# Kernel tuning notes

Hardware: AMD Instinct MI355X
Metric: run time of the kernel (lower is better)

The kernel has to match this reference:

```python
import itertools
import jax, jax.numpy as jnp
import numpy as np

DIM = 448
HEADS = 8
KEY_DIM = 32
ATTN_RATIO = 4
RES = 7
N = RES * RES  # 49 tokens
D_V = KEY_DIM * ATTN_RATIO  # 128
DH = D_V * HEADS  # 1024
H_QKV = DH + 2 * KEY_DIM * HEADS  # 1536
HIDDEN = 4 * DIM  # 1792
SCALE = KEY_DIM ** -0.5
LS_INIT = 1e-05
B = 1024


def _build_bias_idx():
    points = list(itertools.product(range(RES), range(RES)))
    offsets = {}
    idxs = []
    for p1 in points:
        for p2 in points:
            off = (abs(p1[0] - p2[0]), abs(p1[1] - p2[1]))
            if off not in offsets:
                offsets[off] = len(offsets)
            idxs.append(offsets[off])
    return np.array(idxs, dtype=np.int32).reshape(N, N), len(offsets)


def setup_inputs() -> dict:
    key = jax.random.key(0)
    ks = jax.random.split(key, 16)
    bias_idx_np, n_off = _build_bias_idx()
    s = lambda fan: 1.0 / np.sqrt(fan)
    return {
        "x": jax.random.normal(ks[0], (B, N, DIM), jnp.float32),
        "qkv_w": jax.random.normal(ks[1], (H_QKV, DIM), jnp.float32) * s(DIM),
        "qkv_b": jnp.zeros((H_QKV,), jnp.float32),
        "proj_w": jax.random.normal(ks[2], (DIM, DH), jnp.float32) * s(DH),
        "proj_b": jnp.zeros((DIM,), jnp.float32),
        "fc1_w": jax.random.normal(ks[3], (HIDDEN, DIM), jnp.float32) * s(DIM),
        "fc1_b": jnp.zeros((HIDDEN,), jnp.float32),
        "fc2_w": jax.random.normal(ks[4], (DIM, HIDDEN), jnp.float32) * s(HIDDEN),
        "fc2_b": jnp.zeros((DIM,), jnp.float32),
        "norm1_g": jnp.ones((DIM,), jnp.float32),
        "norm1_b": jnp.zeros((DIM,), jnp.float32),
        "norm2_g": jnp.ones((DIM,), jnp.float32),
        "norm2_b": jnp.zeros((DIM,), jnp.float32),
        "ls1_gamma": jnp.full((DIM,), LS_INIT, jnp.float32),
        "ls2_gamma": jnp.full((DIM,), LS_INIT, jnp.float32),
        "attn_biases": jax.random.normal(ks[5], (HEADS, n_off), jnp.float32) * 0.02,
        "bias_idx": jnp.asarray(bias_idx_np),
    }


def _ln(x, g, b, eps=1e-5):
    mu = jnp.mean(x, axis=-1, keepdims=True)
    var = jnp.mean(jnp.square(x - mu), axis=-1, keepdims=True)
    return (x - mu) * jax.lax.rsqrt(var + eps) * g + b


def reference(x, qkv_w, qkv_b, proj_w, proj_b, fc1_w, fc1_b, fc2_w, fc2_b,
              norm1_g, norm1_b, norm2_g, norm2_b, ls1_gamma, ls2_gamma,
              attn_biases, bias_idx):
    Bk, Nk, C = x.shape
    # --- token mixer: attention with gathered relative-position bias ---
    h = _ln(x, norm1_g, norm1_b)
    qkv = (h @ qkv_w.T + qkv_b).reshape(Bk, Nk, HEADS, -1)
    q, k, v = jnp.split(qkv, [KEY_DIM, 2 * KEY_DIM], axis=3)
    # scores: [B, H, N, N]
    attn = jnp.einsum('bnhd,bmhd->bhnm', q, k) * SCALE
    attn = attn + attn_biases[:, bias_idx]  # gather bias [H, N, N]
    attn = jax.nn.softmax(attn, axis=-1)
    out = jnp.einsum('bhnm,bmhd->bnhd', attn, v).reshape(Bk, Nk, DH)
    out = out @ proj_w.T + proj_b
    x = x + out * ls1_gamma
    # --- MLP ---
    h2 = _ln(x, norm2_g, norm2_b)
    h2 = jax.nn.gelu(h2 @ fc1_w.T + fc1_b, approximate=False)
    h2 = h2 @ fc2_w.T + fc2_b
    x = x + h2 * ls2_gamma
    return x
```

## Files before the change

### kernel.cpp

```cpp
#include <hip/hip_runtime.h>
#include <hip/hip_bf16.h>
#include <hip/hip_fp8.h>


#define NTOK 49
#define CDIM 448
#define NHEAD 8
#define DHID 1024
#define HQKV 1536
#define FHID 1792
#define QK_SCALE 0.1767766952966369f
#define INV_SCALE 5.656854249492381f

typedef __attribute__((ext_vector_type(8))) short bf16x8;
typedef __attribute__((ext_vector_type(4))) float f32x4;
typedef unsigned int u32;
typedef unsigned char u8;

__device__ __forceinline__ short f2b(float f) {
    __hip_bfloat16 h = __float2bfloat16(f);
    return *reinterpret_cast<short*>(&h);
}
__device__ __forceinline__ u8 f2f8(float f) {
    __hip_fp8_e4m3 h(f);
    return *reinterpret_cast<u8*>(&h);
}

__device__ __forceinline__ void gll16(const void* g, void* l) {
    __builtin_amdgcn_global_load_lds(
        (const __attribute__((address_space(1))) u32*)g,
        (__attribute__((address_space(3))) u32*)l, 16, 0, 0);
}

__global__ __launch_bounds__(256) void convert_w(
    const float* __restrict__ s0, const float* __restrict__ s1,
    const float* __restrict__ s2, const float* __restrict__ s3,
    u8* __restrict__ d0, u8* __restrict__ d1,
    u8* __restrict__ d2, u8* __restrict__ d3,
    const float* __restrict__ biases, const int* __restrict__ bidx,
    float* __restrict__ bfull)
{
    int i = blockIdx.x * 256 + threadIdx.x;
    if (i < 688128) d0[i] = f2f8(s0[i]);
    if (i < 458752) d1[i] = f2f8(s1[i]);
    if (i < 802816) { d2[i] = f2f8(s2[i]);
                      d3[i] = f2f8(s3[i]); }
    if (i < NHEAD * NTOK * NTOK) {
        int h = i / (NTOK * NTOK), p = i % (NTOK * NTOK);
        bfull[i] = biases[h * NTOK + bidx[p]];
    }
}

__global__ __launch_bounds__(256) void ln_kernel(
    const float* __restrict__ x, u8* __restrict__ out,
    const float* __restrict__ g, const float* __restrict__ b)
{
    int row = blockIdx.x * 4 + (threadIdx.x >> 6);
    int lane = threadIdx.x & 63;
    const float* xr = x + (size_t)row * CDIM;
    float v[7];
    float s = 0.f;
#pragma unroll
    for (int i = 0; i < 7; i++) { v[i] = xr[i * 64 + lane]; s += v[i]; }
#pragma unroll
    for (int o = 32; o > 0; o >>= 1) s += __shfl_xor(s, o, 64);
    float mean = s * (1.0f / 448.0f);
    float q = 0.f;
#pragma unroll
    for (int i = 0; i < 7; i++) { float d = v[i] - mean; q += d * d; }
#pragma unroll
    for (int o = 32; o > 0; o >>= 1) q += __shfl_xor(q, o, 64);
    float rstd = rsqrtf(q * (1.0f / 448.0f) + 1e-5f);
    u8* orow = out + (size_t)row * CDIM;
#pragma unroll
    for (int i = 0; i < 7; i++) {
        int c = i * 64 + lane;
        orow[c] = f2f8((v[i] - mean) * rstd * g[c] + b[c]);
    }
}

template <int EPI>
__global__ __launch_bounds__(256, 4) void gemm_bt(
    const u8* __restrict__ A,
    const u8* __restrict__ W,
    const float* __restrict__ bias,
    const float* __restrict__ ls,
    const float* resid,
    float* outF,
    void* outX,
    int M, int N, int K)
{
    __shared__ __align__(16) u8 sA[3][4096];
    __shared__ __align__(16) u8 sB[3][4096];
    const int tid = threadIdx.x;
    const int lane = tid & 63;
    const int w = tid >> 6;
    const int lr = lane & 15, lq = lane >> 4;

    const int gx = gridDim.x;
    const int nwg = gx * gridDim.y;
    const int lin = blockIdx.y * gx + blockIdx.x;
    const int q8 = nwg >> 3, r8 = nwg & 7;
    const int xcd = lin & 7, sub = lin >> 3;
    const int wg = (xcd < r8 ? xcd * (q8 + 1) : r8 * (q8 + 1) + (xcd - r8) * q8) + sub;
    const int m0 = (wg / gx) * 128;
    const int n0 = (wg % gx) * 128;

    const int sp = lane >> 5;
    const int sh = (lane >> 4) & 1;
    const int sr = lane & 15;
    int rA = m0 + (2 * w + sp) * 16 + sr;
    int rB = n0 + (2 * w + sp) * 16 + sr; rB = rB < N ? rB : N - 1;
    u32 oA = (u32)rA * (u32)K + (u32)(sh * 16);
    u32 oB = (u32)rB * (u32)K + (u32)(sh * 16);
    const int dst = w * 1024;

    const f32x4 fz = {0.f, 0.f, 0.f, 0.f};
    f32x4 acc[4][4];
#pragma unroll
    for (int i = 0; i < 4; i++)
#pragma unroll
        for (int j = 0; j < 4; j++) acc[i][j] = fz;

    const int rdA = (w & 1) * 2048 + (lq >> 1) * 256 + lr * 16 + (lq & 1) * 8;
    const int rdB = (w >> 1) * 2048 + (lq >> 1) * 256 + lr * 16 + (lq & 1) * 8;

    const int nt = K >> 5;
    gll16(A + oA, sA[0] + dst); gll16(W + oB, sB[0] + dst); oA += 32; oB += 32;
    gll16(A + oA, sA[1] + dst); gll16(W + oB, sB[1] + dst); oA += 32; oB += 32;

    int bc = 0;
    int bs = 2;
    for (int t = 0; t < nt; t++) {
        if (t + 1 < nt) asm volatile("s_waitcnt vmcnt(2)" ::: "memory");
        else            asm volatile("s_waitcnt vmcnt(0)" ::: "memory");
        __builtin_amdgcn_s_barrier();
        if (t + 2 < nt) {
            gll16(A + oA, sA[bs] + dst);
            gll16(W + oB, sB[bs] + dst);
            oA += 32; oB += 32;
            bs = (bs == 2) ? 0 : bs + 1;
        }
        const u8* baseA = sA[bc] + rdA;
        const u8* baseB = sB[bc] + rdB;
        bc = (bc == 2) ? 0 : bc + 1;
        long af[4], bfr[4];
#pragma unroll
        for (int i = 0; i < 4; i++) af[i] = *(const long*)(baseA + i * 512);
#pragma unroll
        for (int j = 0; j < 4; j++) bfr[j] = *(const long*)(baseB + j * 512);
#pragma unroll
        for (int i = 0; i < 4; i++)
#pragma unroll
            for (int j = 0; j < 4; j++)
                acc[i][j] = __builtin_amdgcn_mfma_f32_16x16x32_fp8_fp8(
                    af[i], bfr[j], acc[i][j], 0, 0, 0);
    }

    const int wm = (w & 1) * 64, wn = (w >> 1) * 64;
#pragma unroll
    for (int i = 0; i < 4; i++)
#pragma unroll
        for (int j = 0; j < 4; j++)
#pragma unroll
            for (int r = 0; r < 4; r++) {
                int row = m0 + wm + i * 16 + lq * 4 + r;
                int col = n0 + wn + j * 16 + lr;
                if (col < N) {
                    float v = acc[i][j][r] + bias[col];
                    if (EPI == 0) {
                        ((short*)outX)[(size_t)row * N + col] = f2b(v);
                    } else if (EPI == 1) {
                        float gl = v / (1.0f + __expf(-1.702f * v));
                        ((u8*)outX)[(size_t)row * N + col] = f2f8(gl);
                    } else {
                        outF[(size_t)row * N + col] =
                            resid[(size_t)row * N + col] + v * ls[col];
                    }
                }
            }
}

__global__ __launch_bounds__(64) void attn_mfma(
    const short* __restrict__ qkv,
    const float* __restrict__ bfull,
    u8* __restrict__ attn_out)
{
    __shared__ short sP[64 * 72];
    const int head = blockIdx.x;
    const size_t base = (size_t)blockIdx.y * NTOK;
    const int lane = threadIdx.x;
    const int lr = lane & 15, lq = lane >> 4;

    f32x4 sc[4][4];
#pragma unroll
    for (int i = 0; i < 4; i++)
#pragma unroll
        for (int j = 0; j < 4; j++)
#pragma unroll
            for (int r = 0; r < 4; r++) {
                int row = i * 16 + lq * 4 + r, col = j * 16 + lr;
                float v;
                if (col >= NTOK)      v = -1e30f;
                else if (row < NTOK)  v = bfull[head * (NTOK * NTOK) + row * NTOK + col] * INV_SCALE;
                else                  v = 0.f;
                sc[i][j][r] = v;
            }

    bf16x8 qf[4], kf[4];
#pragma unroll
    for (int i = 0; i < 4; i++) {
        int r = i * 16 + lr; r = r < NTOK ? r : NTOK - 1;
        const short* rp = qkv + (base + r) * HQKV + head * 192;
        qf[i] = *(const bf16x8*)(rp + lq * 8);
        kf[i] = *(const bf16x8*)(rp + 32 + lq * 8);
    }
#pragma unroll
    for (int i = 0; i < 4; i++)
#pragma unroll
        for (int j = 0; j < 4; j++)
            sc[i][j] = __builtin_amdgcn_mfma_f32_16x16x32_bf16(
                qf[i], kf[j], sc[i][j], 0, 0, 0);

#pragma unroll
    for (int i = 0; i < 4; i++)
#pragma unroll
        for (int r = 0; r < 4; r++) {
            float s0 = sc[i][0][r] * QK_SCALE;
            float s1 = sc[i][1][r] * QK_SCALE;
            float s2 = sc[i][2][r] * QK_SCALE;
            float s3 = sc[i][3][r] * QK_SCALE;
            float m = fmaxf(fmaxf(s0, s1), fmaxf(s2, s3));
#pragma unroll
            for (int o = 1; o < 16; o <<= 1) m = fmaxf(m, __shfl_xor(m, o, 64));
            float e0 = __expf(s0 - m), e1 = __expf(s1 - m);
            float e2 = __expf(s2 - m), e3 = __expf(s3 - m);
            float l = e0 + e1 + e2 + e3;
#pragma unroll
            for (int o = 1; o < 16; o <<= 1) l += __shfl_xor(l, o, 64);
            float inv = 1.0f / l;
            short* pr = &sP[(i * 16 + lq * 4 + r) * 72];
            pr[lr]      = f2b(e0 * inv);
            pr[16 + lr] = f2b(e1 * inv);
            pr[32 + lr] = f2b(e2 * inv);
            pr[48 + lr] = f2b(e3 * inv);
        }

    bf16x8 pa[4][2];
#pragma unroll
    for (int i = 0; i < 4; i++)
#pragma unroll
        for (int kk = 0; kk < 2; kk++)
            pa[i][kk] = *(const bf16x8*)&sP[(i * 16 + lr) * 72 + kk * 32 + lq * 8];

#pragma unroll
    for (int half = 0; half < 2; half++) {
        const f32x4 fz = {0.f, 0.f, 0.f, 0.f};
        f32x4 o[4][4];
        bf16x8 pb[4][2];
#pragma unroll
        for (int j = 0; j < 4; j++)
#pragma unroll
            for (int kk = 0; kk < 2; kk++) {
                const int d = half * 64 + j * 16 + lr;
                const short* vcol = qkv + head * 192 + 64 + d;
                bf16x8 tvec;
#pragma unroll
                for (int e = 0; e < 8; e++) {
                    int tok = kk * 32 + lq * 8 + e;
                    tvec[e] = tok < NTOK ? vcol[(base + tok) * HQKV] : (short)0;
                }
                pb[j][kk] = tvec;
            }
#pragma unroll
        for (int i = 0; i < 4; i++)
#pragma unroll
            for (int j = 0; j < 4; j++) {
                o[i][j] = __builtin_amdgcn_mfma_f32_16x16x32_bf16(
                    pa[i][0], pb[j][0], fz, 0, 0, 0);
                o[i][j] = __builtin_amdgcn_mfma_f32_16x16x32_bf16(
                    pa[i][1], pb[j][1], o[i][j], 0, 0, 0);
            }
#pragma unroll
        for (int i = 0; i < 4; i++)
#pragma unroll
            for (int j = 0; j < 4; j++)
#pragma unroll
                for (int r = 0; r < 4; r++) {
                    int row = i * 16 + lq * 4 + r;
                    if (row < NTOK)
                        attn_out[(base + row) * DHID + head * 128 + half * 64 + j * 16 + lr] =
                            f2f8(o[i][j][r]);
                }
    }
}

extern "C" void kernel_launch(void* const* d_in, const int* in_sizes, int n_in,
                              void* d_out, int out_size, void* d_ws, size_t ws_size,
                              hipStream_t stream) {
    const float* x      = (const float*)d_in[0];
    const float* qkv_w  = (const float*)d_in[1];
    const float* qkv_b  = (const float*)d_in[2];
    const float* proj_w = (const float*)d_in[3];
    const float* proj_b = (const float*)d_in[4];
    const float* fc1_w  = (const float*)d_in[5];
    const float* fc1_b  = (const float*)d_in[6];
    const float* fc2_w  = (const float*)d_in[7];
    const float* fc2_b  = (const float*)d_in[8];
    const float* n1g    = (const float*)d_in[9];
    const float* n1b    = (const float*)d_in[10];
    const float* n2g    = (const float*)d_in[11];
    const float* n2b    = (const float*)d_in[12];
    const float* ls1    = (const float*)d_in[13];
    const float* ls2    = (const float*)d_in[14];
    const float* biases = (const float*)d_in[15];
    const int*   bidx   = (const int*)d_in[16];
    float* outp = (float*)d_out;

    char* ws = (char*)d_ws;
    u8* Wq = (u8*)ws; ws += 688128;
    u8* Wp = (u8*)ws; ws += 458752;
    u8* W1 = (u8*)ws; ws += 802816;
    u8* W2 = (u8*)ws; ws += 802816;
    float* bfull = (float*)ws; ws += (size_t)NHEAD * NTOK * NTOK * 4;
    const size_t fixed = 2752512 + (size_t)NHEAD * NTOK * NTOK * 4;

    int IC = 1024;
    while (IC > 128) {
        size_t Rr = (size_t)IC * NTOK;
        if (fixed + Rr * 4544ull <= ws_size) break;
        IC >>= 1;
    }
    const size_t R = (size_t)IC * NTOK;
    u8*    hbuf = (u8*)ws;    ws += R * CDIM;
    short* qkvb = (short*)ws; ws += R * HQKV * 2;
    u8*    attb = (u8*)ws;    ws += R * DHID;
    u8*    gbuf = (u8*)qkvb;

    convert_w<<<3136, 256, 0, stream>>>(qkv_w, proj_w, fc1_w, fc2_w,
                                        Wq, Wp, W1, W2, biases, bidx, bfull);

    for (int c0 = 0; c0 < 1024; c0 += IC) {
        const float* xc = x + (size_t)c0 * NTOK * CDIM;
        float* oc = outp + (size_t)c0 * NTOK * CDIM;
        const int Ri = IC * NTOK;
        const int gy = (Ri + 127) / 128;

        ln_kernel<<<Ri / 4, 256, 0, stream>>>(xc, hbuf, n1g, n1b);
        gemm_bt<0><<<dim3(HQKV / 128, gy), 256, 0, stream>>>(
            hbuf, Wq, qkv_b, nullptr, nullptr, nullptr, (void*)qkvb, Ri, HQKV, CDIM);
        attn_mfma<<<dim3(NHEAD, IC), 64, 0, stream>>>(qkvb, bfull, attb);
        gemm_bt<2><<<dim3(4, gy), 256, 0, stream>>>(
            attb, Wp, proj_b, ls1, xc, oc, nullptr, Ri, CDIM, DHID);
        ln_kernel<<<Ri / 4, 256, 0, stream>>>(oc, hbuf, n2g, n2b);
        gemm_bt<1><<<dim3(FHID / 128, gy), 256, 0, stream>>>(
            hbuf, W1, fc1_b, nullptr, nullptr, nullptr, (void*)gbuf, Ri, FHID, CDIM);
        gemm_bt<2><<<dim3(4, gy), 256, 0, stream>>>(
            gbuf, W2, fc2_b, ls2, oc, oc, nullptr, Ri, CDIM, FHID);
    }
}
```

Baseline: 788.9 us.

## Pre-pack FP8 GEMM operands into MFMA tile layout and raise MFMA priority

All FP8 GEMM operands (weights, LN outputs, attention output, GELU output) are now written in a blocked 16-row by 32-k tile layout. Each global_load_lds then copies one contiguous 512-byte chunk per 16-row group instead of strided 16-byte pieces from separate rows, and LDS reads become simple contiguous 8-byte fragments. The producer kernels now do scattered byte writes with extra index math. The MFMA loop is also bracketed with s_setprio to favour matrix issue.

```diff
diff --git a/kernel.cpp b/kernel.cpp
--- a/kernel.cpp
+++ b/kernel.cpp
@@ -24,6 +24,11 @@
 __device__ __forceinline__ u8 f2f8(float f) {
     __hip_fp8_e4m3 h(f);
     return *reinterpret_cast<u8*>(&h);
+}
+
+__device__ __forceinline__ u32 pack_off(int row, int k, int nkp) {
+    return (u32)(((row >> 4) * nkp + (k >> 5)) << 9) +
+           (u32)((((k & 31) >> 3) << 7) + ((row & 15) << 3) + (k & 7));
 }
 
 __device__ __forceinline__ void gll16(const void* g, void* l) {
@@ -41,10 +46,20 @@
     float* __restrict__ bfull)
 {
     int i = blockIdx.x * 256 + threadIdx.x;
-    if (i < 688128) d0[i] = f2f8(s0[i]);
-    if (i < 458752) d1[i] = f2f8(s1[i]);
-    if (i < 802816) { d2[i] = f2f8(s2[i]);
-                      d3[i] = f2f8(s3[i]); }
+    if (i < 688128) {
+        int n = i / 448, k = i - n * 448;
+        d0[pack_off(n, k, 14)] = f2f8(s0[i]);
+    }
+    if (i < 458752) {
+        int n = i >> 10, k = i & 1023;
+        d1[pack_off(n, k, 32)] = f2f8(s1[i]);
+    }
+    if (i < 802816) {
+        int n2 = i / 448, k2 = i - n2 * 448;
+        d2[pack_off(n2, k2, 14)] = f2f8(s2[i]);
+        int n3 = i / 1792, k3 = i - n3 * 1792;
+        d3[pack_off(n3, k3, 56)] = f2f8(s3[i]);
+    }
     if (i < NHEAD * NTOK * NTOK) {
         int h = i / (NTOK * NTOK), p = i % (NTOK * NTOK);
         bfull[i] = biases[h * NTOK + bidx[p]];
@@ -71,11 +86,10 @@
 #pragma unroll
     for (int o = 32; o > 0; o >>= 1) q += __shfl_xor(q, o, 64);
     float rstd = rsqrtf(q * (1.0f / 448.0f) + 1e-5f);
-    u8* orow = out + (size_t)row * CDIM;
 #pragma unroll
     for (int i = 0; i < 7; i++) {
         int c = i * 64 + lane;
-        orow[c] = f2f8((v[i] - mean) * rstd * g[c] + b[c]);
+        out[pack_off(row, c, 14)] = f2f8((v[i] - mean) * rstd * g[c] + b[c]);
     }
 }
 
@@ -106,13 +120,13 @@
     const int m0 = (wg / gx) * 128;
     const int n0 = (wg % gx) * 128;
 
-    const int sp = lane >> 5;
-    const int sh = (lane >> 4) & 1;
-    const int sr = lane & 15;
-    int rA = m0 + (2 * w + sp) * 16 + sr;
-    int rB = n0 + (2 * w + sp) * 16 + sr; rB = rB < N ? rB : N - 1;
-    u32 oA = (u32)rA * (u32)K + (u32)(sh * 16);
-    u32 oB = (u32)rB * (u32)K + (u32)(sh * 16);
+    const int nkp = K >> 5;
+    const int maxpB = (N >> 4) - 1;
+    int prA = (m0 >> 4) + 2 * w + (lane >> 5);
+    int prB = (n0 >> 4) + 2 * w + (lane >> 5);
+    prB = prB < maxpB ? prB : maxpB;
+    u32 oA = (u32)(prA * nkp) * 512u + (u32)((lane & 31) * 16);
+    u32 oB = (u32)(prB * nkp) * 512u + (u32)((lane & 31) * 16);
     const int dst = w * 1024;
 
     const f32x4 fz = {0.f, 0.f, 0.f, 0.f};
@@ -122,12 +136,12 @@
 #pragma unroll
         for (int j = 0; j < 4; j++) acc[i][j] = fz;
 
-    const int rdA = (w & 1) * 2048 + (lq >> 1) * 256 + lr * 16 + (lq & 1) * 8;
-    const int rdB = (w >> 1) * 2048 + (lq >> 1) * 256 + lr * 16 + (lq & 1) * 8;
+    const int rdA = (w & 1) * 2048 + lq * 128 + lr * 8;
+    const int rdB = (w >> 1) * 2048 + lq * 128 + lr * 8;
 
     const int nt = K >> 5;
-    gll16(A + oA, sA[0] + dst); gll16(W + oB, sB[0] + dst); oA += 32; oB += 32;
-    gll16(A + oA, sA[1] + dst); gll16(W + oB, sB[1] + dst); oA += 32; oB += 32;
+    gll16(A + oA, sA[0] + dst); gll16(W + oB, sB[0] + dst); oA += 512; oB += 512;
+    gll16(A + oA, sA[1] + dst); gll16(W + oB, sB[1] + dst); oA += 512; oB += 512;
 
     int bc = 0;
     int bs = 2;
@@ -138,7 +152,7 @@
         if (t + 2 < nt) {
             gll16(A + oA, sA[bs] + dst);
             gll16(W + oB, sB[bs] + dst);
-            oA += 32; oB += 32;
+            oA += 512; oB += 512;
             bs = (bs == 2) ? 0 : bs + 1;
         }
         const u8* baseA = sA[bc] + rdA;
@@ -149,12 +163,14 @@
         for (int i = 0; i < 4; i++) af[i] = *(const long*)(baseA + i * 512);
 #pragma unroll
         for (int j = 0; j < 4; j++) bfr[j] = *(const long*)(baseB + j * 512);
+        __builtin_amdgcn_s_setprio(1);
 #pragma unroll
         for (int i = 0; i < 4; i++)
 #pragma unroll
             for (int j = 0; j < 4; j++)
                 acc[i][j] = __builtin_amdgcn_mfma_f32_16x16x32_fp8_fp8(
                     af[i], bfr[j], acc[i][j], 0, 0, 0);
+        __builtin_amdgcn_s_setprio(0);
     }
 
     const int wm = (w & 1) * 64, wn = (w >> 1) * 64;
@@ -172,7 +188,7 @@
                         ((short*)outX)[(size_t)row * N + col] = f2b(v);
                     } else if (EPI == 1) {
                         float gl = v / (1.0f + __expf(-1.702f * v));
-                        ((u8*)outX)[(size_t)row * N + col] = f2f8(gl);
+                        ((u8*)outX)[pack_off(row, col, N >> 5)] = f2f8(gl);
                     } else {
                         outF[(size_t)row * N + col] =
                             resid[(size_t)row * N + col] + v * ls[col];
@@ -289,7 +305,8 @@
                 for (int r = 0; r < 4; r++) {
                     int row = i * 16 + lq * 4 + r;
                     if (row < NTOK)
-                        attn_out[(base + row) * DHID + head * 128 + half * 64 + j * 16 + lr] =
+                        attn_out[pack_off((int)(base + row),
+                                          head * 128 + half * 64 + j * 16 + lr, 32)] =
                             f2f8(o[i][j][r]);
                 }
     }
```

Measured after the change: 736.8 us. 6.6% less time.
